# Kernel optimization log

Hardware: AMD Instinct MI355X
Metric: run time of the kernel (lower is better)

The kernel has to match this reference:

```python
import jax, jax.numpy as jnp
import numpy as np

# Config mirrors TACO_hashed init: data_size=[1024,1024], dimensions=[[4]*5,[4]*5]
N = 262144          # number of query coordinates
DH = 256            # dim_hidden
TD = 4              # tile_dim = dimensions[0][0]
NLEV = 5            # n_levels
W0C = 30.0          # w0
DIMS = np.array([[4]*NLEV, [4]*NLEV])                 # [2, n_levels]
CUM = 1024 // np.cumprod(DIMS, axis=1)                # cum_bases per axis, [2, n_levels]


def setup_inputs() -> dict:
    key = jax.random.key(0)
    ks = jax.random.split(key, 9)
    s = 1.0 / np.sqrt(DH)
    e = TD * TD  # embedding dim = tile_dim**2 = 16
    return {
        "coords": jax.random.randint(ks[0], (N, 2), 0, 1024, dtype=jnp.int32),
        "W0": jax.random.normal(ks[1], (2, DH), jnp.float32) * (1.0 / np.sqrt(2.0)),
        "b0": jnp.zeros((DH,), jnp.float32),
        "Wh": jax.random.normal(ks[2], (3, DH, DH), jnp.float32) * s,  # hidden SIREN linears
        "bh": jnp.zeros((3, DH), jnp.float32),
        "emb": jax.random.normal(ks[3], (NLEV - 1, e, e), jnp.float32),      # per-level embedding tables
        "modW": jax.random.normal(ks[4], (NLEV - 1, e, DH), jnp.float32) * (1.0 / np.sqrt(e)),  # modulator linears (no bias)
        "Wl": jax.random.normal(ks[5], (DH, 3), jnp.float32) * s,  # last_layer
        "bl": jnp.zeros((3,), jnp.float32),
    }


def reference(coords, W0, b0, Wh, bh, emb, modW, Wl, bl):
    dims = jnp.asarray(DIMS.T)   # [n_levels, 2]
    cum = jnp.asarray(CUM.T)     # [n_levels, 2]
    # decompose_coords: per-level bitwise-style div/mod  -> [N, n_levels, 2]
    lv = (coords[:, None, :] // cum[None]) % dims[None]
    # modulator indices for levels 1..n_levels-1: idx = y*tile_dim + x  -> [N, n_levels-1]
    idx = lv[:, 1:, 1] * TD + lv[:, 1:, 0]
    # SIREN input is level-0 coords as float (faithful to the source)
    x = lv[:, 0, :].astype(jnp.float32) @ W0 + b0
    x = x + W0C * (emb[0][idx[:, 0]] @ modW[0])
    x = jnp.sin(W0C * x)
    for j in range(3):
        x = x @ Wh[j] + bh[j]
        x = x + W0C * (emb[j + 1][idx[:, j + 1]] @ modW[j + 1])
        x = jnp.sin(W0C * x)
    return x @ Wl + bl
```

## Files before the change

### kernel.cpp

```cpp
#include <hip/hip_runtime.h>
#include <hip/hip_bf16.h>
#include <math.h>


typedef float  f32x4  __attribute__((ext_vector_type(4)));
typedef int    i32x4  __attribute__((ext_vector_type(4)));
typedef __bf16 bf16x8 __attribute__((ext_vector_type(8)));

__device__ __forceinline__ float fbar(float v) {
  asm volatile("" : "+v"(v));
  return v;
}

__device__ __forceinline__ unsigned short f2bf_rne(float x) {
  unsigned u = __float_as_uint(x);
  unsigned r = (u + 0x7fffu + ((u >> 16) & 1u)) >> 16;
  return (unsigned short)r;
}

__device__ __forceinline__ float sin30(float x) {
  const float Ch = 4.774648189544678f;
  const float Cl = 1.0321218e-07f;
  float revh = x * Ch;
  fbar(revh);
  float e    = __builtin_fmaf(x, Ch, -revh);
  float revl = __builtin_fmaf(x, Cl, e);
  float k2   = __builtin_rintf(revh + revh);
  float g    = __builtin_fmaf(k2, -0.5f, revh) + revl;
  float g2 = g * g;
  float r = -15.0946f;
  r = __builtin_fmaf(r, g2, 42.0601f);
  r = __builtin_fmaf(r, g2, -76.70585f);
  r = __builtin_fmaf(r, g2, 81.6052492f);
  r = __builtin_fmaf(r, g2, -41.341702f);
  r = __builtin_fmaf(r, g2, 6.2831853f);
  float s = g * r;
  int ki = (int)k2;
  return __uint_as_float(__float_as_uint(s) ^ ((unsigned)(ki & 1) << 31));
}

__device__ __forceinline__ void sincos30(float x, float* so, float* co) {
  const float Ch = 4.774648189544678f;
  const float Cl = 1.0321218e-07f;
  float revh = x * Ch;
  fbar(revh);
  float e    = __builtin_fmaf(x, Ch, -revh);
  float revl = __builtin_fmaf(x, Cl, e);
  float k2   = __builtin_rintf(revh + revh);
  float g    = __builtin_fmaf(k2, -0.5f, revh) + revl;
  float u = g * g;
  float sr = -15.0946f;
  sr = __builtin_fmaf(sr, u, 42.0601f);
  sr = __builtin_fmaf(sr, u, -76.70585f);
  sr = __builtin_fmaf(sr, u, 81.6052492f);
  sr = __builtin_fmaf(sr, u, -41.341702f);
  sr = __builtin_fmaf(sr, u, 6.2831853f);
  float s = g * sr;
  float cr = -26.4259f;
  cr = __builtin_fmaf(cr, u, 60.2446f);
  cr = __builtin_fmaf(cr, u, -85.4568f);
  cr = __builtin_fmaf(cr, u, 64.9393940f);
  cr = __builtin_fmaf(cr, u, -19.7392088f);
  float c = __builtin_fmaf(cr, u, 1.0f);
  int ki = (int)k2;
  unsigned sgn = ((unsigned)(ki & 1)) << 31;
  *so = __uint_as_float(__float_as_uint(s) ^ sgn);
  *co = __uint_as_float(__float_as_uint(c) ^ sgn);
}

__global__ void k_prep(const float* __restrict__ emb, const float* __restrict__ modW,
                       float* __restrict__ Mf, const float* __restrict__ W2,
                       unsigned short* __restrict__ B2T) {
  int b = blockIdx.x, d = threadIdx.x;
  if (b < 64) {
    int j = b >> 4, i = b & 15;
    float acc = 0.0f;
#pragma unroll
    for (int e = 0; e < 16; ++e)
      acc = __builtin_fmaf(emb[j * 256 + i * 16 + e], modW[(j * 16 + e) * 256 + d], acc);
    Mf[b * 256 + d] = acc;
  } else {
    int col = b - 64, k = d;
    float w = W2[k * 256 + col];
    unsigned short hi = f2bf_rne(w);
    float hif = __uint_as_float((unsigned)hi << 16);
    unsigned short lo = f2bf_rne(w - hif);
    B2T[col * 768 + k] = hi;
    B2T[col * 768 + 256 + k] = lo;
    B2T[col * 768 + 512 + k] = hi;
  }
}

__global__ void k_prep2(const float* __restrict__ Mf3, const float* __restrict__ Wl,
                        unsigned* __restrict__ B2u) {
  int col = blockIdx.x, d = threadIdx.x;
  int i3 = col / 3, q = col - 3 * (col / 3);
  float pm = fbar(30.0f * Mf3[i3 * 256 + d]);
  float s, c;
  sincos30(pm, &s, &c);
  float w = Wl[d * 3 + q];
  unsigned ts = (unsigned)f2bf_rne(s * w);
  unsigned tc = (unsigned)f2bf_rne(c * w);
  B2u[col * 256 + d] = (tc << 16) | ts;
}

__global__ void __launch_bounds__(256) k_h123(
    const float* __restrict__ W0, const float* __restrict__ b0,
    const float* __restrict__ Wh0, const float* __restrict__ bh0,
    const float* __restrict__ W1, const float* __restrict__ b1,
    const float* __restrict__ Mf,
    unsigned short* __restrict__ Ah, unsigned short* __restrict__ Al) {
  __shared__ float xs1[256];
  __shared__ float xs2[4][256];
  int b = blockIdx.x, d = threadIdx.x;
  int c1 = b >> 2;
  float lvx = (float)((c1 >> 6) & 3), lvy = (float)((c1 >> 4) & 3);
  int i0 = c1 & 15;
  float t = fbar(lvx * W0[d]);
  t = __builtin_fmaf(lvy, W0[256 + d], t);
  t = fbar(t + b0[d]);
  float p = fbar(30.0f * Mf[i0 * 256 + d]);
  float xv = fbar(t + p);
  xs1[d] = sinf(fbar(30.0f * xv));
  __syncthreads();
  float acc = 0.0f;
  for (int k = 0; k < 256; ++k)
    acc = __builtin_fmaf(xs1[k], Wh0[k * 256 + d], acc);
  float t2 = fbar(acc + bh0[d]);
#pragma unroll
  for (int r = 0; r < 4; ++r) {
    int i1 = 4 * (b & 3) + r;
    float pp = fbar(30.0f * Mf[4096 + i1 * 256 + d]);
    float x2 = fbar(t2 + pp);
    xs2[r][d] = sinf(fbar(30.0f * x2));
  }
  __syncthreads();
  float m2[16];
#pragma unroll
  for (int i = 0; i < 16; ++i) m2[i] = fbar(30.0f * Mf[8192 + i * 256 + d]);
  float acc3[4];
#pragma unroll
  for (int r = 0; r < 4; ++r) acc3[r] = 0.0f;
  for (int k = 0; k < 256; ++k) {
    float w = W1[k * 256 + d];
#pragma unroll
    for (int r = 0; r < 4; ++r) acc3[r] = __builtin_fmaf(xs2[r][k], w, acc3[r]);
  }
  float bias = b1[d];
#pragma unroll
  for (int r = 0; r < 4; ++r) {
    float tr = fbar(acc3[r] + bias);
    int c3base = (b * 4 + r) * 16;
#pragma unroll
    for (int i = 0; i < 16; ++i) {
      float x = fbar(tr + m2[i]);
      float h = sin30(x);
      unsigned short hi = f2bf_rne(h);
      float hif = __uint_as_float((unsigned)hi << 16);
      unsigned short lo = f2bf_rne(h - hif);
      size_t o = (size_t)(c3base + i) * 256 + d;
      Ah[o] = hi;
      Al[o] = lo;
    }
  }
}

__global__ void __launch_bounds__(512, 1) k_gemm(
    const unsigned short* __restrict__ Ah, const unsigned short* __restrict__ Al,
    const unsigned short* __restrict__ B2T, const float* __restrict__ b2,
    unsigned* __restrict__ SC) {
  __shared__ unsigned short As[128 * 40];
  __shared__ unsigned short Bs[256 * 40];
  const int t = threadIdx.x;
  const int lane = t & 63, wid = t >> 6;
  const int l15 = lane & 15, l4 = lane >> 4;
  const int wm = (wid >> 2) * 64;
  const int wn = (wid & 3) * 64;
  const size_t r0 = (size_t)blockIdx.x * 128;

  const int s_arow = t >> 2, s_apart = t & 3;
  const int s_bcol0 = t >> 2, s_bcol1 = 128 + (t >> 2), s_bpart = t & 3;

  f32x4 acc[4][4];
#pragma unroll
  for (int rf = 0; rf < 4; ++rf)
#pragma unroll
    for (int cf = 0; cf < 4; ++cf) acc[rf][cf] = (f32x4){0.f, 0.f, 0.f, 0.f};

  i32x4 ra, rb0, rb1;
  ra  = *(const i32x4*)(Ah + ((r0 + s_arow) << 8) + s_apart * 8);
  rb0 = *(const i32x4*)(B2T + s_bcol0 * 768 + s_bpart * 8);
  rb1 = *(const i32x4*)(B2T + s_bcol1 * 768 + s_bpart * 8);

#pragma unroll 1
  for (int c = 0; c < 24; ++c) {
    *(i32x4*)(As + s_arow * 40 + s_apart * 8) = ra;
    *(i32x4*)(Bs + s_bcol0 * 40 + s_bpart * 8) = rb0;
    *(i32x4*)(Bs + s_bcol1 * 40 + s_bpart * 8) = rb1;
    __syncthreads();
    if (c < 23) {
      int cn = c + 1;
      int kk = cn & 7;
      const unsigned short* asrc = (cn >= 16) ? Al : Ah;
      ra  = *(const i32x4*)(asrc + ((r0 + s_arow) << 8) + kk * 32 + s_apart * 8);
      rb0 = *(const i32x4*)(B2T + s_bcol0 * 768 + cn * 32 + s_bpart * 8);
      rb1 = *(const i32x4*)(B2T + s_bcol1 * 768 + cn * 32 + s_bpart * 8);
    }
    bf16x8 af[4], bfr[4];
#pragma unroll
    for (int rf = 0; rf < 4; ++rf)
      af[rf] = __builtin_bit_cast(
          bf16x8, *(const i32x4*)(As + (wm + rf * 16 + l15) * 40 + l4 * 8));
#pragma unroll
    for (int cf = 0; cf < 4; ++cf)
      bfr[cf] = __builtin_bit_cast(
          bf16x8, *(const i32x4*)(Bs + (wn + cf * 16 + l15) * 40 + l4 * 8));
#pragma unroll
    for (int rf = 0; rf < 4; ++rf)
#pragma unroll
      for (int cf = 0; cf < 4; ++cf)
        acc[rf][cf] = __builtin_amdgcn_mfma_f32_16x16x32_bf16(
            af[rf], bfr[cf], acc[rf][cf], 0, 0, 0);
    __syncthreads();
  }

#pragma unroll
  for (int cf = 0; cf < 4; ++cf) {
    float bias = b2[wn + cf * 16 + l15];
#pragma unroll
    for (int rf = 0; rf < 4; ++rf) {
      size_t rbase = r0 + wm + rf * 16 + l4 * 4;
#pragma unroll
      for (int j = 0; j < 4; ++j) {
        float g = acc[rf][cf][j] + bias;
        float s, c;
        sincos30(g, &s, &c);
        unsigned pk = ((unsigned)f2bf_rne(s) << 16) | (unsigned)f2bf_rne(c);
        SC[(rbase + j) * 256 + wn + cf * 16 + l15] = pk;
      }
    }
  }
}

__global__ void __launch_bounds__(512, 1) k_ugemm(
    const unsigned short* __restrict__ SCb, const unsigned* __restrict__ B2u,
    float* __restrict__ U) {
  __shared__ unsigned short As[128 * 40];
  __shared__ unsigned Bs[48 * 260];
  const int t = threadIdx.x;
  const int lane = t & 63, wid = t >> 6;
  const int l15 = lane & 15, l4 = lane >> 4;
  const int wm = wid * 16;
  const size_t r0 = (size_t)blockIdx.x * 128;

#pragma unroll
  for (int i = 0; i < 24; ++i) {
    int lin = t + i * 512;
    int col = lin >> 8, kp = lin & 255;
    Bs[col * 260 + kp] = B2u[lin];
  }

  const int s_row = t >> 2, s_part = t & 3;
  f32x4 acc[3];
#pragma unroll
  for (int cf = 0; cf < 3; ++cf) acc[cf] = (f32x4){0.f, 0.f, 0.f, 0.f};

  i32x4 ra = *(const i32x4*)(SCb + (r0 + s_row) * 512 + s_part * 8);
#pragma unroll 1
  for (int c = 0; c < 16; ++c) {
    *(i32x4*)(As + s_row * 40 + s_part * 8) = ra;
    __syncthreads();
    if (c < 15)
      ra = *(const i32x4*)(SCb + (r0 + s_row) * 512 + (c + 1) * 32 + s_part * 8);
    bf16x8 af = __builtin_bit_cast(
        bf16x8, *(const i32x4*)(As + (wm + l15) * 40 + l4 * 8));
#pragma unroll
    for (int cf = 0; cf < 3; ++cf) {
      bf16x8 bfr = __builtin_bit_cast(
          bf16x8, *(const i32x4*)(Bs + (cf * 16 + l15) * 260 + c * 16 + l4 * 4));
      acc[cf] = __builtin_amdgcn_mfma_f32_16x16x32_bf16(af, bfr, acc[cf], 0, 0, 0);
    }
    __syncthreads();
  }

#pragma unroll
  for (int cf = 0; cf < 3; ++cf) {
    size_t rbase = r0 + wm + l4 * 4;
#pragma unroll
    for (int j = 0; j < 4; ++j)
      U[(rbase + j) * 48 + cf * 16 + l15] = acc[cf][j];
  }
}

__global__ void k_gather(const int* __restrict__ coords, const float* __restrict__ U,
                         const float* __restrict__ bl, float* __restrict__ out, int N) {
  int n = blockIdx.x * blockDim.x + threadIdx.x;
  if (n >= N) return;
  int x = coords[2 * n], y = coords[2 * n + 1];
  int c1 = ((x >> 8) & 3) * 64 + ((y >> 8) & 3) * 16 +
           (((y >> 6) & 3) * 4 + ((x >> 6) & 3));
  int i1 = ((y >> 4) & 3) * 4 + ((x >> 4) & 3);
  int i2 = ((y >> 2) & 3) * 4 + ((x >> 2) & 3);
  int i3 = (y & 3) * 4 + (x & 3);
  int c3 = (c1 * 16 + i1) * 16 + i2;
  const float* up = U + (size_t)c3 * 48 + i3 * 3;
  out[n * 3 + 0] = up[0] + bl[0];
  out[n * 3 + 1] = up[1] + bl[1];
  out[n * 3 + 2] = up[2] + bl[2];
}

__global__ void k_direct(const int* __restrict__ coords, const float* __restrict__ W0,
                         const float* __restrict__ b0, const float* __restrict__ Wh,
                         const float* __restrict__ bh, const float* __restrict__ emb,
                         const float* __restrict__ modW, const float* __restrict__ Wl,
                         const float* __restrict__ bl, float* __restrict__ out) {
  __shared__ float xs[256];
  __shared__ float red[256];
  int n = blockIdx.x, d = threadIdx.x;
  int x = coords[2 * n], y = coords[2 * n + 1];
  float lvx = (float)((x >> 8) & 3), lvy = (float)((y >> 8) & 3);
  int idx[4];
  idx[0] = ((y >> 6) & 3) * 4 + ((x >> 6) & 3);
  idx[1] = ((y >> 4) & 3) * 4 + ((x >> 4) & 3);
  idx[2] = ((y >> 2) & 3) * 4 + ((x >> 2) & 3);
  idx[3] = (y & 3) * 4 + (x & 3);
  float m = 0.0f;
#pragma unroll
  for (int e = 0; e < 16; ++e)
    m = __builtin_fmaf(emb[idx[0] * 16 + e], modW[e * 256 + d], m);
  float t = fbar(lvx * W0[d]);
  t = __builtin_fmaf(lvy, W0[256 + d], t);
  t = fbar(t + b0[d]);
  float p = fbar(30.0f * m);
  float xv = fbar(t + p);
  xs[d] = sinf(fbar(30.0f * xv));
  __syncthreads();
  for (int j = 0; j < 3; ++j) {
    float acc = 0.0f;
    for (int k = 0; k < 256; ++k)
      acc = __builtin_fmaf(xs[k], Wh[j * 65536 + k * 256 + d], acc);
    float tt = fbar(acc + bh[j * 256 + d]);
    m = 0.0f;
#pragma unroll
    for (int e = 0; e < 16; ++e)
      m = __builtin_fmaf(emb[(j + 1) * 256 + idx[j + 1] * 16 + e],
                         modW[((j + 1) * 16 + e) * 256 + d], m);
    p = fbar(30.0f * m);
    xv = fbar(tt + p);
    float h = sinf(fbar(30.0f * xv));
    __syncthreads();
    xs[d] = h;
    __syncthreads();
  }
  for (int q = 0; q < 3; ++q) {
    red[d] = xs[d] * Wl[d * 3 + q];
    __syncthreads();
    for (int s = 128; s > 0; s >>= 1) {
      if (d < s) red[d] += red[d + s];
      __syncthreads();
    }
    if (d == 0) out[n * 3 + q] = red[0] + bl[q];
    __syncthreads();
  }
}

extern "C" void kernel_launch(void* const* d_in, const int* in_sizes, int n_in,
                              void* d_out, int out_size, void* d_ws, size_t ws_size,
                              hipStream_t stream) {
  const int*   coords = (const int*)d_in[0];
  const float* W0   = (const float*)d_in[1];
  const float* b0   = (const float*)d_in[2];
  const float* Wh   = (const float*)d_in[3];
  const float* bh   = (const float*)d_in[4];
  const float* emb  = (const float*)d_in[5];
  const float* modW = (const float*)d_in[6];
  const float* Wl   = (const float*)d_in[7];
  const float* bl   = (const float*)d_in[8];
  float* out = (float*)d_out;
  const int N = in_sizes[0] / 2;

  const size_t OFF_MF  = 0;
  const size_t OFF_B2T = 65536;
  const size_t OFF_AH  = 458752;
  const size_t OFF_AL  = 34013184;
  const size_t OFF_SC  = 67567616;
  const size_t OFF_B2  = 134676480;
  const size_t OFF_U   = OFF_AH;
  const size_t NEED    = 134774784;

  if (ws_size >= NEED) {
    char* ws = (char*)d_ws;
    float*          Mf  = (float*)(ws + OFF_MF);
    unsigned short* B2T = (unsigned short*)(ws + OFF_B2T);
    unsigned short* Ahp = (unsigned short*)(ws + OFF_AH);
    unsigned short* Alp = (unsigned short*)(ws + OFF_AL);
    unsigned*       SC  = (unsigned*)(ws + OFF_SC);
    unsigned*       B2u = (unsigned*)(ws + OFF_B2);
    float*          U   = (float*)(ws + OFF_U);

    k_prep<<<320, 256, 0, stream>>>(emb, modW, Mf, Wh + 131072, B2T);
    k_prep2<<<48, 256, 0, stream>>>(Mf + 12288, Wl, B2u);
    k_h123<<<1024, 256, 0, stream>>>(W0, b0, Wh, bh, Wh + 65536, bh + 256, Mf,
                                     Ahp, Alp);
    k_gemm<<<512, 512, 0, stream>>>(Ahp, Alp, B2T, bh + 512, SC);
    k_ugemm<<<512, 512, 0, stream>>>((const unsigned short*)SC, B2u, U);
    k_gather<<<(N + 255) / 256, 256, 0, stream>>>(coords, U, bl, out, N);
  } else {
    k_direct<<<N, 256, 0, stream>>>(coords, W0, b0, Wh, bh, emb, modW, Wl, bl, out);
  }
}
```

Measured before the change: 113.1 us.

## Double-buffer GEMM tiles via direct global-to-LDS loads and split h123 K across 512 threads

The main GEMM now stages A and B tiles into double-buffered LDS with global_load_lds, removing the register round-trip and one barrier per k-step so loads overlap MFMA work. The LDS row padding goes away (stride 32 instead of 40), which may raise bank conflicts on the fragment reads. k_h123 now runs 512 threads per block and splits the W1 K-loop between two halves, merging partial sums through shared memory. This adds barriers and leaves half the threads idle during the first layer.

```diff
diff --git a/kernel.cpp b/kernel.cpp
--- a/kernel.cpp
+++ b/kernel.cpp
@@ -16,6 +16,12 @@
   unsigned u = __float_as_uint(x);
   unsigned r = (u + 0x7fffu + ((u >> 16) & 1u)) >> 16;
   return (unsigned short)r;
+}
+
+__device__ __forceinline__ void gload16(const void* g, void* l) {
+  __builtin_amdgcn_global_load_lds(
+      (const __attribute__((address_space(1))) unsigned*)g,
+      (__attribute__((address_space(3))) unsigned*)l, 16, 0, 0);
 }
 
 __device__ __forceinline__ float sin30(float x) {
@@ -104,52 +110,80 @@
   B2u[col * 256 + d] = (tc << 16) | ts;
 }
 
-__global__ void __launch_bounds__(256) k_h123(
+__global__ void __launch_bounds__(512) k_h123(
     const float* __restrict__ W0, const float* __restrict__ b0,
     const float* __restrict__ Wh0, const float* __restrict__ bh0,
     const float* __restrict__ W1, const float* __restrict__ b1,
     const float* __restrict__ Mf,
     unsigned short* __restrict__ Ah, unsigned short* __restrict__ Al) {
   __shared__ float xs1[256];
+  __shared__ float t2s[256];
   __shared__ float xs2[4][256];
-  int b = blockIdx.x, d = threadIdx.x;
+  __shared__ float ph[4][256];
+  __shared__ float th[2][256];
+  int b = blockIdx.x, t = threadIdx.x;
+  int d = t & 255, r2 = t >> 8;
   int c1 = b >> 2;
-  float lvx = (float)((c1 >> 6) & 3), lvy = (float)((c1 >> 4) & 3);
-  int i0 = c1 & 15;
-  float t = fbar(lvx * W0[d]);
-  t = __builtin_fmaf(lvy, W0[256 + d], t);
-  t = fbar(t + b0[d]);
-  float p = fbar(30.0f * Mf[i0 * 256 + d]);
-  float xv = fbar(t + p);
-  xs1[d] = sinf(fbar(30.0f * xv));
-  __syncthreads();
-  float acc = 0.0f;
-  for (int k = 0; k < 256; ++k)
-    acc = __builtin_fmaf(xs1[k], Wh0[k * 256 + d], acc);
-  float t2 = fbar(acc + bh0[d]);
-#pragma unroll
-  for (int r = 0; r < 4; ++r) {
+  if (r2 == 0) {
+    float lvx = (float)((c1 >> 6) & 3), lvy = (float)((c1 >> 4) & 3);
+    int i0 = c1 & 15;
+    float tt = fbar(lvx * W0[d]);
+    tt = __builtin_fmaf(lvy, W0[256 + d], tt);
+    tt = fbar(tt + b0[d]);
+    float p = fbar(30.0f * Mf[i0 * 256 + d]);
+    float xv = fbar(tt + p);
+    xs1[d] = sinf(fbar(30.0f * xv));
+  }
+  __syncthreads();
+  if (r2 == 0) {
+    float acc = 0.0f;
+    for (int k = 0; k < 256; ++k)
+      acc = __builtin_fmaf(xs1[k], Wh0[k * 256 + d], acc);
+    t2s[d] = fbar(acc + bh0[d]);
+  }
+  __syncthreads();
+  float t2v = t2s[d];
+#pragma unroll
+  for (int rr = 0; rr < 2; ++rr) {
+    int r = r2 * 2 + rr;
     int i1 = 4 * (b & 3) + r;
     float pp = fbar(30.0f * Mf[4096 + i1 * 256 + d]);
-    float x2 = fbar(t2 + pp);
+    float x2 = fbar(t2v + pp);
     xs2[r][d] = sinf(fbar(30.0f * x2));
   }
   __syncthreads();
   float m2[16];
 #pragma unroll
   for (int i = 0; i < 16; ++i) m2[i] = fbar(30.0f * Mf[8192 + i * 256 + d]);
-  float acc3[4];
-#pragma unroll
-  for (int r = 0; r < 4; ++r) acc3[r] = 0.0f;
-  for (int k = 0; k < 256; ++k) {
+  float acc3[4] = {0.f, 0.f, 0.f, 0.f};
+  int k0 = r2 * 128;
+  for (int k = k0; k < k0 + 128; ++k) {
     float w = W1[k * 256 + d];
 #pragma unroll
     for (int r = 0; r < 4; ++r) acc3[r] = __builtin_fmaf(xs2[r][k], w, acc3[r]);
   }
+  if (r2 == 1) {
+#pragma unroll
+    for (int r = 0; r < 4; ++r) ph[r][d] = acc3[r];
+  }
+  __syncthreads();
+  float tot0, tot1;
+  if (r2 == 0) {
+    tot0 = acc3[0] + ph[0][d];
+    tot1 = acc3[1] + ph[1][d];
+    th[0][d] = acc3[2] + ph[2][d];
+    th[1][d] = acc3[3] + ph[3][d];
+  }
+  __syncthreads();
+  if (r2 == 1) {
+    tot0 = th[0][d];
+    tot1 = th[1][d];
+  }
   float bias = b1[d];
 #pragma unroll
-  for (int r = 0; r < 4; ++r) {
-    float tr = fbar(acc3[r] + bias);
+  for (int rr = 0; rr < 2; ++rr) {
+    int r = r2 * 2 + rr;
+    float tr = fbar((rr ? tot1 : tot0) + bias);
     int c3base = (b * 4 + r) * 16;
 #pragma unroll
     for (int i = 0; i < 16; ++i) {
@@ -169,8 +203,8 @@
     const unsigned short* __restrict__ Ah, const unsigned short* __restrict__ Al,
     const unsigned short* __restrict__ B2T, const float* __restrict__ b2,
     unsigned* __restrict__ SC) {
-  __shared__ unsigned short As[128 * 40];
-  __shared__ unsigned short Bs[256 * 40];
+  __shared__ unsigned short As[2][128 * 32];
+  __shared__ unsigned short Bs[2][256 * 32];
   const int t = threadIdx.x;
   const int lane = t & 63, wid = t >> 6;
   const int l15 = lane & 15, l4 = lane >> 4;
@@ -178,8 +212,8 @@
   const int wn = (wid & 3) * 64;
   const size_t r0 = (size_t)blockIdx.x * 128;
 
-  const int s_arow = t >> 2, s_apart = t & 3;
-  const int s_bcol0 = t >> 2, s_bcol1 = 128 + (t >> 2), s_bpart = t & 3;
+  const int arow = t >> 2, apart = t & 3;
+  const size_t bcol0 = t >> 2, bcol1 = (t >> 2) + 128;
 
   f32x4 acc[4][4];
 #pragma unroll
@@ -187,34 +221,32 @@
 #pragma unroll
     for (int cf = 0; cf < 4; ++cf) acc[rf][cf] = (f32x4){0.f, 0.f, 0.f, 0.f};
 
-  i32x4 ra, rb0, rb1;
-  ra  = *(const i32x4*)(Ah + ((r0 + s_arow) << 8) + s_apart * 8);
-  rb0 = *(const i32x4*)(B2T + s_bcol0 * 768 + s_bpart * 8);
-  rb1 = *(const i32x4*)(B2T + s_bcol1 * 768 + s_bpart * 8);
-
+#define STAGE(c, bb)                                                         \
+  {                                                                          \
+    const unsigned short* asrc = ((c) >= 16) ? Al : Ah;                      \
+    gload16(asrc + ((r0 + arow) << 8) + ((c) & 7) * 32 + apart * 8,          \
+            (void*)(&As[bb][wid * 512]));                                    \
+    gload16(B2T + bcol0 * 768 + (c) * 32 + apart * 8,                        \
+            (void*)(&Bs[bb][wid * 512]));                                    \
+    gload16(B2T + bcol1 * 768 + (c) * 32 + apart * 8,                        \
+            (void*)(&Bs[bb][(wid + 8) * 512]));                              \
+  }
+
+  STAGE(0, 0);
+  __syncthreads();
 #pragma unroll 1
   for (int c = 0; c < 24; ++c) {
-    *(i32x4*)(As + s_arow * 40 + s_apart * 8) = ra;
-    *(i32x4*)(Bs + s_bcol0 * 40 + s_bpart * 8) = rb0;
-    *(i32x4*)(Bs + s_bcol1 * 40 + s_bpart * 8) = rb1;
-    __syncthreads();
-    if (c < 23) {
-      int cn = c + 1;
-      int kk = cn & 7;
-      const unsigned short* asrc = (cn >= 16) ? Al : Ah;
-      ra  = *(const i32x4*)(asrc + ((r0 + s_arow) << 8) + kk * 32 + s_apart * 8);
-      rb0 = *(const i32x4*)(B2T + s_bcol0 * 768 + cn * 32 + s_bpart * 8);
-      rb1 = *(const i32x4*)(B2T + s_bcol1 * 768 + cn * 32 + s_bpart * 8);
-    }
+    int cur = c & 1;
+    if (c < 23) STAGE(c + 1, cur ^ 1);
     bf16x8 af[4], bfr[4];
 #pragma unroll
     for (int rf = 0; rf < 4; ++rf)
       af[rf] = __builtin_bit_cast(
-          bf16x8, *(const i32x4*)(As + (wm + rf * 16 + l15) * 40 + l4 * 8));
+          bf16x8, *(const i32x4*)(&As[cur][(wm + rf * 16 + l15) * 32 + l4 * 8]));
 #pragma unroll
     for (int cf = 0; cf < 4; ++cf)
       bfr[cf] = __builtin_bit_cast(
-          bf16x8, *(const i32x4*)(Bs + (wn + cf * 16 + l15) * 40 + l4 * 8));
+          bf16x8, *(const i32x4*)(&Bs[cur][(wn + cf * 16 + l15) * 32 + l4 * 8]));
 #pragma unroll
     for (int rf = 0; rf < 4; ++rf)
 #pragma unroll
@@ -223,6 +255,7 @@
             af[rf], bfr[cf], acc[rf][cf], 0, 0, 0);
     __syncthreads();
   }
+#undef STAGE
 
 #pragma unroll
   for (int cf = 0; cf < 4; ++cf) {
@@ -400,7 +433,7 @@
 
     k_prep<<<320, 256, 0, stream>>>(emb, modW, Mf, Wh + 131072, B2T);
     k_prep2<<<48, 256, 0, stream>>>(Mf + 12288, Wl, B2u);
-    k_h123<<<1024, 256, 0, stream>>>(W0, b0, Wh, bh, Wh + 65536, bh + 256, Mf,
+    k_h123<<<1024, 512, 0, stream>>>(W0, b0, Wh, bh, Wh + 65536, bh + 256, Mf,
                                      Ahp, Alp);
     k_gemm<<<512, 512, 0, stream>>>(Ahp, Alp, B2T, bh + 512, SC);
     k_ugemm<<<512, 512, 0, stream>>>((const unsigned short*)SC, B2u, U);
```

New measurement: 121.2 us. 1.07x slower.
